# Optimization experiments

Measured on AMD Instinct MI355X. Metric: run time of the kernel, lower is better.

## Reference

```python
import jax, jax.numpy as jnp
import numpy as np

N_NODES = 50000
N_EDGES = 800000
H_NODE = 128
H_EDGE = 128
EPS = 1e-5


def _bn(x, gamma, beta):
    # training-mode BatchNorm1d over axis 0 (biased variance)
    mean = jnp.mean(x, axis=0)
    var = jnp.var(x, axis=0)
    return (x - mean) * jax.lax.rsqrt(var + EPS) * gamma + beta


def setup_inputs() -> dict:
    key = jax.random.key(0)
    ks = jax.random.split(key, 8)
    d_in = H_NODE + H_EDGE          # 256
    d_out = 2 * H_NODE              # 256
    bound = 1.0 / np.sqrt(d_in)
    return {
        "node_emb": jax.random.normal(ks[0], (N_NODES, H_NODE), jnp.float32),
        "edge_emb": jax.random.normal(ks[1], (N_EDGES, H_EDGE), jnp.float32),
        "i": jax.random.randint(ks[2], (N_EDGES,), 0, N_NODES, jnp.int64),
        "w1": jax.random.uniform(ks[3], (d_out, d_in), jnp.float32, -bound, bound),
        "b1": jax.random.uniform(ks[4], (d_out,), jnp.float32, -bound, bound),
        "g1": jnp.ones((d_out,), jnp.float32),
        "be1": jnp.zeros((d_out,), jnp.float32),
        "g2": jnp.ones((H_NODE,), jnp.float32),
        "be2": jnp.zeros((H_NODE,), jnp.float32),
    }


def reference(node_emb, edge_emb, i, w1, b1, g1, be1, g2, be2):
    # gather + concat: [E, H_NODE + H_EDGE]
    c1 = jnp.concatenate([node_emb[i], edge_emb], axis=1)
    # linear -> BN: [E, 2*H_NODE]
    c1 = _bn(c1 @ w1.T + b1, g1, be1)
    c1_filter, c1_core = jnp.split(c1, 2, axis=1)
    msg = jax.nn.sigmoid(c1_filter) * jnp.tanh(c1_core)  # [E, H_NODE]
    # scatter-sum back to nodes
    c1_emb = jax.ops.segment_sum(msg, i, num_segments=node_emb.shape[0])
    c1_emb = _bn(c1_emb, g2, be2)
    return jnp.tanh(node_emb + c1_emb)
```

## Files before the change

kernel.cpp:

```cpp
#include <hip/hip_runtime.h>
#include <hip/hip_fp16.h>
#include <cstdint>
#include <cstddef>

#define NN 50000
#define NE 800000
#define EPSV 1e-5f
#define NTILES (NE / 128)
#define EGRID 768

typedef _Float16 f16_t;
typedef f16_t f16x8 __attribute__((ext_vector_type(8)));
typedef f16_t f16x4 __attribute__((ext_vector_type(4)));
typedef f16_t f16x2 __attribute__((ext_vector_type(2)));
typedef float f32x4 __attribute__((ext_vector_type(4)));

__device__ __forceinline__ float fast_tanh(float x) {
  float e2 = __expf(2.f * x);
  return 1.f - 2.f / (e2 + 1.f);
}
__device__ __forceinline__ float fast_sigmoid(float x) {
  return 1.f / (1.f + __expf(-x));
}

__launch_bounds__(256, 4)
__global__ void node_proj(const float* __restrict__ A, const float* __restrict__ w1,
                          const float* __restrict__ b1, f16_t* __restrict__ P) {
  __shared__ f16_t Alds[128][136];
  const int tid = threadIdx.x;
  const int wave = tid >> 6;
  const int lane = tid & 63;
  const int quad = lane >> 4;
  const int l16 = lane & 15;

  int cols[4];
#pragma unroll
  for (int nt = 0; nt < 4; ++nt) cols[nt] = 16 * wave + 64 * nt + l16;

  f16x8 bfrag[4][4];
#pragma unroll
  for (int nt = 0; nt < 4; ++nt)
#pragma unroll
    for (int ks = 0; ks < 4; ++ks) {
      const float* src = w1 + (size_t)cols[nt] * 256 + ks * 32 + quad * 8;
#pragma unroll
      for (int j = 0; j < 8; ++j) bfrag[nt][ks][j] = (f16_t)src[j];
    }

  float c0[4];
#pragma unroll
  for (int nt = 0; nt < 4; ++nt) c0[nt] = b1[cols[nt]];

  const int row0 = blockIdx.x * 128;
  {
    const int r = tid >> 1, half = tid & 1;
    const int grow = row0 + r;
    f16_t* dst = &Alds[r][half * 64];
    if (grow < NN) {
      const float4* src = (const float4*)(A + (size_t)grow * 128 + half * 64);
#pragma unroll
      for (int c = 0; c < 8; ++c) {
        float4 v0 = src[2 * c], v1 = src[2 * c + 1];
        f16x8 pk = {(f16_t)v0.x, (f16_t)v0.y, (f16_t)v0.z, (f16_t)v0.w,
                    (f16_t)v1.x, (f16_t)v1.y, (f16_t)v1.z, (f16_t)v1.w};
        *(f16x8*)(dst + c * 8) = pk;
      }
    } else {
      f16x8 z = {0, 0, 0, 0, 0, 0, 0, 0};
#pragma unroll
      for (int c = 0; c < 8; ++c) *(f16x8*)(dst + c * 8) = z;
    }
  }
  __syncthreads();

#pragma unroll 1
  for (int m = 0; m < 8; ++m) {
    f16x8 afrag[4];
#pragma unroll
    for (int ks = 0; ks < 4; ++ks)
      afrag[ks] = *(const f16x8*)&Alds[m * 16 + l16][ks * 32 + quad * 8];
    f32x4 acc[4];
#pragma unroll
    for (int nt = 0; nt < 4; ++nt) acc[nt] = (f32x4){0.f, 0.f, 0.f, 0.f};
#pragma unroll
    for (int ks = 0; ks < 4; ++ks)
#pragma unroll
      for (int nt = 0; nt < 4; ++nt)
        acc[nt] = __builtin_amdgcn_mfma_f32_16x16x32_f16(
            afrag[ks], bfrag[nt][ks], acc[nt], 0, 0, 0);
    const int rbase = row0 + m * 16 + quad * 4;
#pragma unroll
    for (int reg = 0; reg < 4; ++reg) {
      int g = rbase + reg;
      if (g < NN) {
        f16x2 pA, pB;
        pA[0] = (f16_t)(acc[0][reg] + c0[0]);
        pA[1] = (f16_t)(acc[2][reg] + c0[2]);
        pB[0] = (f16_t)(acc[1][reg] + c0[1]);
        pB[1] = (f16_t)(acc[3][reg] + c0[3]);
        *(f16x2*)&P[(size_t)g * 256 + wave * 32 + l16 * 2] = pA;
        *(f16x2*)&P[(size_t)g * 256 + (wave + 4) * 32 + l16 * 2] = pB;
      }
    }
  }
}

template <int MODE>
__launch_bounds__(512, 6)
__global__ void edge_pass(const float* __restrict__ A, const float* __restrict__ w1,
                          const int* __restrict__ idx, const f16_t* __restrict__ P,
                          float* __restrict__ stats, const float* __restrict__ st,
                          f16_t* __restrict__ outp, int* __restrict__ ctr) {
  __shared__ f16_t Alds[128][136];
  __shared__ int sIdx[128];
  __shared__ int s_tile;
  const int tid = threadIdx.x;
  const int w = tid >> 6;
  const int lane = tid & 63;
  const int quad = lane >> 4;
  const int l16 = lane & 15;

  int cols[2];
#pragma unroll
  for (int n = 0; n < 2; ++n) cols[n] = 16 * w + 128 * n + l16;

  f16x8 bfrag[2][4];
#pragma unroll
  for (int n = 0; n < 2; ++n)
#pragma unroll
    for (int ks = 0; ks < 4; ++ks) {
      const float* src = w1 + (size_t)cols[n] * 256 + 128 + ks * 32 + quad * 8;
#pragma unroll
      for (int j = 0; j < 8; ++j) bfrag[n][ks][j] = (f16_t)src[j];
    }

  float c0[2], c1c[2];
  if (MODE == 2) {
#pragma unroll
    for (int n = 0; n < 2; ++n) {
      c0[n] = st[cols[n]];
      c1c[n] = st[256 + cols[n]];
    }
  }
  float ssum[2] = {0.f, 0.f};
  float ssq[2] = {0.f, 0.f};

  for (;;) {
    if (tid == 0) s_tile = atomicAdd(ctr, 1);
    __syncthreads();
    const int t = s_tile;
    if (t >= NTILES) break;
    const int row0 = t * 128;

    if (tid < 128) sIdx[tid] = idx[row0 + tid];
    {
      const int r = tid >> 2, q4 = tid & 3;
      const float4* src = (const float4*)(A + (size_t)(row0 + r) * 128 + q4 * 32);
      f16_t* dst = &Alds[r][q4 * 32];
#pragma unroll
      for (int c = 0; c < 4; ++c) {
        float4 v0 = src[2 * c], v1 = src[2 * c + 1];
        f16x8 pk = {(f16_t)v0.x, (f16_t)v0.y, (f16_t)v0.z, (f16_t)v0.w,
                    (f16_t)v1.x, (f16_t)v1.y, (f16_t)v1.z, (f16_t)v1.w};
        *(f16x8*)(dst + c * 8) = pk;
      }
    }
    __syncthreads();

    int nodeC[4];
    f16x2 pvC[4];
#pragma unroll
    for (int reg = 0; reg < 4; ++reg) {
      nodeC[reg] = sIdx[quad * 4 + reg];
      pvC[reg] = *(const f16x2*)&P[(size_t)nodeC[reg] * 256 + w * 32 + l16 * 2];
    }

#pragma unroll 1
    for (int m = 0; m < 8; ++m) {
      const int mm = (m + 1) & 7;
      int nodeN[4];
      f16x2 pvN[4];
#pragma unroll
      for (int reg = 0; reg < 4; ++reg) {
        nodeN[reg] = sIdx[mm * 16 + quad * 4 + reg];
        pvN[reg] = *(const f16x2*)&P[(size_t)nodeN[reg] * 256 + w * 32 + l16 * 2];
      }

      f16x8 afrag[4];
#pragma unroll
      for (int ks = 0; ks < 4; ++ks)
        afrag[ks] = *(const f16x8*)&Alds[m * 16 + l16][ks * 32 + quad * 8];

      f32x4 acc[2];
      acc[0] = (f32x4){0.f, 0.f, 0.f, 0.f};
      acc[1] = (f32x4){0.f, 0.f, 0.f, 0.f};
      __builtin_amdgcn_s_setprio(1);
#pragma unroll
      for (int ks = 0; ks < 4; ++ks) {
        acc[0] = __builtin_amdgcn_mfma_f32_16x16x32_f16(afrag[ks], bfrag[0][ks],
                                                        acc[0], 0, 0, 0);
        acc[1] = __builtin_amdgcn_mfma_f32_16x16x32_f16(afrag[ks], bfrag[1][ks],
                                                        acc[1], 0, 0, 0);
      }
      __builtin_amdgcn_s_setprio(0);

#pragma unroll
      for (int reg = 0; reg < 4; ++reg) {
        const float h0 = acc[0][reg] + (float)pvC[reg][0];
        const float h1 = acc[1][reg] + (float)pvC[reg][1];
        if (MODE == 2) {
          const float hn0 = h0 * c0[0] + c1c[0];
          const float hn1 = h1 * c0[1] + c1c[1];
          const float msg = fast_sigmoid(hn0) * fast_tanh(hn1);
          const float o = __shfl_xor(msg, 1);
          if ((l16 & 1) == 0) {
            f16x2 val;
            val[0] = (f16_t)msg;
            val[1] = (f16_t)o;
            __half2* addr =
                (__half2*)&outp[(size_t)nodeC[reg] * 128 + 16 * w + (l16 & ~1)];
            unsafeAtomicAdd(addr, *(__half2*)&val);
          }
        } else {
          ssum[0] += h0; ssq[0] += h0 * h0;
          ssum[1] += h1; ssq[1] += h1 * h1;
          if (MODE == 3) {
            f16x2 hp = {(f16_t)h0, (f16_t)h1};
            const int edge = row0 + m * 16 + quad * 4 + reg;
            *(f16x2*)&outp[(size_t)edge * 256 + w * 32 + l16 * 2] = hp;
          }
        }
      }
#pragma unroll
      for (int reg = 0; reg < 4; ++reg) {
        nodeC[reg] = nodeN[reg];
        pvC[reg] = pvN[reg];
      }
    }
    __syncthreads();
  }

  if (MODE != 2) {
#pragma unroll
    for (int n = 0; n < 2; ++n) {
      float s = ssum[n], q = ssq[n];
      s += __shfl_xor(s, 16); s += __shfl_xor(s, 32);
      q += __shfl_xor(q, 16); q += __shfl_xor(q, 32);
      if (quad == 0) {
        atomicAdd(&stats[cols[n]], s);
        atomicAdd(&stats[256 + cols[n]], q);
      }
    }
  }
}

__global__ void finalize1(const float* __restrict__ stats, const float* __restrict__ g1,
                          const float* __restrict__ be1, float* __restrict__ st,
                          float* __restrict__ st_sw) {
  int j = threadIdx.x;
  float mean = stats[j] * (1.f / NE);
  float var = stats[256 + j] * (1.f / NE) - mean * mean;
  float s = g1[j] * rsqrtf(var + EPSV);
  float t = be1[j] - mean * s;
  st[j] = s;
  st[256 + j] = t;
  int wq = (j >> 4) & 7, n = j >> 7, lj = j & 15;
  int pos = wq * 32 + lj * 2 + n;
  st_sw[pos] = s;
  st_sw[256 + pos] = t;
}

__launch_bounds__(256, 8)
__global__ void edge_apply(const f16_t* __restrict__ hsw, const int* __restrict__ idx,
                           const float* __restrict__ stw, f16_t* __restrict__ acc16) {
  const int i = blockIdx.x * 256 + threadIdx.x;
  const int e = i >> 5;
  const int k2 = i & 31;
  const int node = idx[e];
  const int w = k2 >> 3, lp = k2 & 7;
  const f16x4 ha = *(const f16x4*)&hsw[(size_t)e * 256 + w * 32 + lp * 4];
  const f16x4 hb = *(const f16x4*)&hsw[(size_t)e * 256 + (w + 4) * 32 + lp * 4];
  const float4 sA = *(const float4*)&stw[w * 32 + lp * 4];
  const float4 sB = *(const float4*)&stw[(w + 4) * 32 + lp * 4];
  const float4 tA = *(const float4*)&stw[256 + w * 32 + lp * 4];
  const float4 tB = *(const float4*)&stw[256 + (w + 4) * 32 + lp * 4];
  f16x2 va, vb;
  va[0] = (f16_t)(fast_sigmoid((float)ha[0] * sA.x + tA.x) *
                  fast_tanh((float)ha[1] * sA.y + tA.y));
  va[1] = (f16_t)(fast_sigmoid((float)ha[2] * sA.z + tA.z) *
                  fast_tanh((float)ha[3] * sA.w + tA.w));
  vb[0] = (f16_t)(fast_sigmoid((float)hb[0] * sB.x + tB.x) *
                  fast_tanh((float)hb[1] * sB.y + tB.y));
  vb[1] = (f16_t)(fast_sigmoid((float)hb[2] * sB.z + tB.z) *
                  fast_tanh((float)hb[3] * sB.w + tB.w));
  const int cA = 16 * w + 2 * lp;
  f16_t* rowp = acc16 + (size_t)node * 128;
  unsafeAtomicAdd((__half2*)(rowp + cA), *(__half2*)&va);
  unsafeAtomicAdd((__half2*)(rowp + 64 + cA), *(__half2*)&vb);
}

__global__ void bn2_stats(const f16_t* __restrict__ acc16, float* __restrict__ stats) {
  const int tid = threadIdx.x;
  const int c2 = tid & 63;
  const int ph = tid >> 6;
  float s0 = 0.f, s1 = 0.f, q0 = 0.f, q1 = 0.f;
  for (int row = blockIdx.x * 4 + ph; row < NN; row += gridDim.x * 4) {
    f16x2 v = *(const f16x2*)&acc16[(size_t)row * 128 + 2 * c2];
    float a = (float)v[0], b = (float)v[1];
    s0 += a; q0 += a * a;
    s1 += b; q1 += b * b;
  }
  __shared__ float red[256][4];
  red[tid][0] = s0; red[tid][1] = s1; red[tid][2] = q0; red[tid][3] = q1;
  __syncthreads();
  if (ph == 0) {
    float a0 = 0.f, a1 = 0.f, b0 = 0.f, b1 = 0.f;
#pragma unroll
    for (int p = 0; p < 4; ++p) {
      a0 += red[p * 64 + c2][0]; a1 += red[p * 64 + c2][1];
      b0 += red[p * 64 + c2][2]; b1 += red[p * 64 + c2][3];
    }
    atomicAdd(&stats[2 * c2], a0);
    atomicAdd(&stats[2 * c2 + 1], a1);
    atomicAdd(&stats[128 + 2 * c2], b0);
    atomicAdd(&stats[128 + 2 * c2 + 1], b1);
  }
}

__global__ void final_kernel(const float* __restrict__ node_emb,
                             const float* __restrict__ bn2sums,
                             const float* __restrict__ g2, const float* __restrict__ be2,
                             const f16_t* __restrict__ acc16, float* __restrict__ out) {
  int i = blockIdx.x * blockDim.x + threadIdx.x;
  if (i >= NN * 32) return;
  int c4 = i & 31;
  int row = i >> 5;
  float4 sm = ((const float4*)bn2sums)[c4];
  float4 sq = ((const float4*)(bn2sums + 128))[c4];
  float4 g = ((const float4*)g2)[c4];
  float4 b = ((const float4*)be2)[c4];
  float4 s4, h4;
  {
    float mean, var;
    mean = sm.x * (1.f / NN); var = sq.x * (1.f / NN) - mean * mean;
    s4.x = g.x * rsqrtf(var + EPSV); h4.x = b.x - mean * s4.x;
    mean = sm.y * (1.f / NN); var = sq.y * (1.f / NN) - mean * mean;
    s4.y = g.y * rsqrtf(var + EPSV); h4.y = b.y - mean * s4.y;
    mean = sm.z * (1.f / NN); var = sq.z * (1.f / NN) - mean * mean;
    s4.z = g.z * rsqrtf(var + EPSV); h4.z = b.z - mean * s4.z;
    mean = sm.w * (1.f / NN); var = sq.w * (1.f / NN) - mean * mean;
    s4.w = g.w * rsqrtf(var + EPSV); h4.w = b.w - mean * s4.w;
  }
  float4 ne = ((const float4*)node_emb)[i];
  f16x4 cv = *(const f16x4*)&acc16[(size_t)row * 128 + c4 * 4];
  float4 r;
  r.x = fast_tanh(ne.x + (float)cv[0] * s4.x + h4.x);
  r.y = fast_tanh(ne.y + (float)cv[1] * s4.y + h4.y);
  r.z = fast_tanh(ne.z + (float)cv[2] * s4.z + h4.z);
  r.w = fast_tanh(ne.w + (float)cv[3] * s4.w + h4.w);
  ((float4*)out)[i] = r;
}

extern "C" void kernel_launch(void* const* d_in, const int* in_sizes, int n_in,
                              void* d_out, int out_size, void* d_ws, size_t ws_size,
                              hipStream_t stream) {
  (void)in_sizes; (void)n_in; (void)out_size;
  const float* node_emb = (const float*)d_in[0];
  const float* edge_emb = (const float*)d_in[1];
  const int* idx = (const int*)d_in[2];
  const float* w1 = (const float*)d_in[3];
  const float* b1 = (const float*)d_in[4];
  const float* g1 = (const float*)d_in[5];
  const float* be1 = (const float*)d_in[6];
  const float* g2 = (const float*)d_in[7];
  const float* be2 = (const float*)d_in[8];
  float* out = (float*)d_out;

  float* wsf = (float*)d_ws;
  float* bn1sums = wsf;
  float* st = wsf + 512;
  float* bn2sums = wsf + 1024;
  int* ctr1 = (int*)(wsf + 1536);
  int* ctr2 = (int*)(wsf + 1537);
  float* st_sw = wsf + 2048;
  char* base = (char*)d_ws + 16384;
  f16_t* P = (f16_t*)base;
  f16_t* acc16 = (f16_t*)(base + (size_t)NN * 512);
  f16_t* hsw = (f16_t*)(base + (size_t)NN * 512 + (size_t)NN * 256);
  const size_t need_h = 16384 + (size_t)NN * 512 + (size_t)NN * 256 + (size_t)NE * 512;

  hipMemsetAsync(wsf, 0, 2560 * sizeof(float), stream);
  hipMemsetAsync(acc16, 0, (size_t)NN * 256, stream);

  node_proj<<<(NN + 127) / 128, 256, 0, stream>>>(node_emb, w1, b1, P);
  if (ws_size >= need_h) {
    edge_pass<3><<<EGRID, 512, 0, stream>>>(edge_emb, w1, idx, P, bn1sums, nullptr,
                                            hsw, ctr1);
    finalize1<<<1, 256, 0, stream>>>(bn1sums, g1, be1, st, st_sw);
    edge_apply<<<NE * 32 / 256, 256, 0, stream>>>(hsw, idx, st_sw, acc16);
  } else {
    edge_pass<1><<<EGRID, 512, 0, stream>>>(edge_emb, w1, idx, P, bn1sums, nullptr,
                                            nullptr, ctr1);
    finalize1<<<1, 256, 0, stream>>>(bn1sums, g1, be1, st, st_sw);
    edge_pass<2><<<EGRID, 512, 0, stream>>>(edge_emb, w1, idx, P, bn1sums, st,
                                            acc16, ctr2);
  }
  bn2_stats<<<256, 256, 0, stream>>>(acc16, bn2sums);
  final_kernel<<<(NN * 32 + 255) / 256, 256, 0, stream>>>(node_emb, bn2sums, g2,
                                                          be2, acc16, out);
}
```

Baseline: 911.7 us.

## Replace atomic scatter with CSR-grouped segment reduction into LDS

Builds a CSR edge list sorted by destination node (count, single-block scan, fill) and adds an apply2 kernel where each block owns 64 nodes, gathers their edges' pre-BN activations, applies BN, gate and tanh, and accumulates into shared memory before writing fp16 results once. This is meant to remove global atomic scatter contention and the acc16 memset. In exchange it adds three small kernels plus a serial 1024-thread scan, irregular gathers of hsw rows, and load imbalance across nodes. The path is only taken when the workspace is large enough.

After: 1.176 ms. +29.0%, slower.

```diff
diff --git a/kernel.cpp b/kernel.cpp
--- a/kernel.cpp
+++ b/kernel.cpp
@@ -8,6 +8,8 @@
 #define EPSV 1e-5f
 #define NTILES (NE / 128)
 #define EGRID 768
+#define SCAN_T 1024
+#define CHUNK ((NN + SCAN_T - 1) / SCAN_T)
 
 typedef _Float16 f16_t;
 typedef f16_t f16x8 __attribute__((ext_vector_type(8)));
@@ -57,10 +59,10 @@
     const int grow = row0 + r;
     f16_t* dst = &Alds[r][half * 64];
     if (grow < NN) {
-      const float4* src = (const float4*)(A + (size_t)grow * 128 + half * 64);
+      const f32x4* src = (const f32x4*)(A + (size_t)grow * 128 + half * 64);
 #pragma unroll
       for (int c = 0; c < 8; ++c) {
-        float4 v0 = src[2 * c], v1 = src[2 * c + 1];
+        f32x4 v0 = src[2 * c], v1 = src[2 * c + 1];
         f16x8 pk = {(f16_t)v0.x, (f16_t)v0.y, (f16_t)v0.z, (f16_t)v0.w,
                     (f16_t)v1.x, (f16_t)v1.y, (f16_t)v1.z, (f16_t)v1.w};
         *(f16x8*)(dst + c * 8) = pk;
@@ -155,11 +157,11 @@
     if (tid < 128) sIdx[tid] = idx[row0 + tid];
     {
       const int r = tid >> 2, q4 = tid & 3;
-      const float4* src = (const float4*)(A + (size_t)(row0 + r) * 128 + q4 * 32);
+      const f32x4* src = (const f32x4*)(A + (size_t)(row0 + r) * 128 + q4 * 32);
       f16_t* dst = &Alds[r][q4 * 32];
 #pragma unroll
       for (int c = 0; c < 4; ++c) {
-        float4 v0 = src[2 * c], v1 = src[2 * c + 1];
+        f32x4 v0 = src[2 * c], v1 = src[2 * c + 1];
         f16x8 pk = {(f16_t)v0.x, (f16_t)v0.y, (f16_t)v0.z, (f16_t)v0.w,
                     (f16_t)v1.x, (f16_t)v1.y, (f16_t)v1.z, (f16_t)v1.w};
         *(f16x8*)(dst + c * 8) = pk;
@@ -268,6 +270,116 @@
   int pos = wq * 32 + lj * 2 + n;
   st_sw[pos] = s;
   st_sw[256 + pos] = t;
+}
+
+__global__ void csr_count(const int* __restrict__ idx, int* __restrict__ cnt) {
+  int i = blockIdx.x * 256 + threadIdx.x;
+  if (i < NE / 4) {
+    int4 v = ((const int4*)idx)[i];
+    atomicAdd(&cnt[v.x], 1);
+    atomicAdd(&cnt[v.y], 1);
+    atomicAdd(&cnt[v.z], 1);
+    atomicAdd(&cnt[v.w], 1);
+  }
+}
+
+__global__ void csr_scan(const int* __restrict__ cnt, int* __restrict__ off,
+                         int* __restrict__ cur) {
+  __shared__ int ls[SCAN_T];
+  const int t = threadIdx.x;
+  const int b0 = t * CHUNK;
+  int s = 0;
+  for (int k = 0; k < CHUNK; ++k) {
+    int n = b0 + k;
+    if (n < NN) s += cnt[n];
+  }
+  ls[t] = s;
+  __syncthreads();
+  for (int d = 1; d < SCAN_T; d <<= 1) {
+    int u = (t >= d) ? ls[t - d] : 0;
+    __syncthreads();
+    ls[t] += u;
+    __syncthreads();
+  }
+  int run = ls[t] - s;
+  for (int k = 0; k < CHUNK; ++k) {
+    int n = b0 + k;
+    if (n < NN) {
+      off[n] = run;
+      cur[n] = run;
+      run += cnt[n];
+    }
+  }
+  if (t == SCAN_T - 1) off[NN] = run;
+}
+
+__global__ void csr_fill(const int* __restrict__ idx, int* __restrict__ cur,
+                         int* __restrict__ elist) {
+  int i = blockIdx.x * 256 + threadIdx.x;
+  if (i < NE / 4) {
+    int4 v = ((const int4*)idx)[i];
+    int e = 4 * i;
+    elist[atomicAdd(&cur[v.x], 1)] = (e)     | ((v.x & 63) << 20);
+    elist[atomicAdd(&cur[v.y], 1)] = (e + 1) | ((v.y & 63) << 20);
+    elist[atomicAdd(&cur[v.z], 1)] = (e + 2) | ((v.z & 63) << 20);
+    elist[atomicAdd(&cur[v.w], 1)] = (e + 3) | ((v.w & 63) << 20);
+  }
+}
+
+__launch_bounds__(256, 4)
+__global__ void apply2(const f16_t* __restrict__ hsw, const int* __restrict__ off,
+                       const int* __restrict__ elist, const float* __restrict__ stw,
+                       f16_t* __restrict__ acc16) {
+  __shared__ float accL[64 * 128];
+  const int tid = threadIdx.x;
+  const int wv = tid >> 6;
+  const int lane = tid & 63;
+  const int n0 = blockIdx.x * 64;
+
+  for (int i = tid; i < 64 * 128; i += 256) accL[i] = 0.f;
+
+  const float4 sv = *(const float4*)&stw[lane * 4];
+  const float4 tv = *(const float4*)&stw[256 + lane * 4];
+  const int c0 = 16 * (lane >> 3) + ((lane & 7) << 1);
+  __syncthreads();
+
+  int na = n0 + 16 * wv;
+  int nb = na + 16;
+  if (na > NN) na = NN;
+  if (nb > NN) nb = NN;
+  const int jbeg = (na <= NN) ? off[na] : NE;
+  const int jend = (nb <= NN) ? off[nb] : NE;
+
+  for (int jb = jbeg; jb < jend; jb += 64) {
+    const int nent = (jend - jb < 64) ? (jend - jb) : 64;
+    int ent = (jb + lane < jend) ? elist[jb + lane] : 0;
+#pragma unroll 4
+    for (int j = 0; j < nent; ++j) {
+      const int en = __shfl(ent, j);
+      const int e = en & 0xFFFFF;
+      const int ln = en >> 20;
+      const f16x4 h = *(const f16x4*)&hsw[(size_t)e * 256 + lane * 4];
+      const float m0 = fast_sigmoid((float)h[0] * sv.x + tv.x) *
+                       fast_tanh((float)h[1] * sv.y + tv.y);
+      const float m1 = fast_sigmoid((float)h[2] * sv.z + tv.z) *
+                       fast_tanh((float)h[3] * sv.w + tv.w);
+      float* p = &accL[ln * 128 + c0];
+      p[0] += m0;
+      p[1] += m1;
+    }
+  }
+  __syncthreads();
+
+  const int cp = tid & 63;
+  const int g = tid >> 6;
+  for (int r = g * 16; r < g * 16 + 16; ++r) {
+    const int n = n0 + r;
+    if (n >= NN) break;
+    f16x2 o;
+    o[0] = (f16_t)accL[r * 128 + 2 * cp];
+    o[1] = (f16_t)accL[r * 128 + 2 * cp + 1];
+    *(f16x2*)&acc16[(size_t)n * 128 + 2 * cp] = o;
+  }
 }
 
 __launch_bounds__(256, 8)
@@ -387,18 +499,34 @@
   f16_t* P = (f16_t*)base;
   f16_t* acc16 = (f16_t*)(base + (size_t)NN * 512);
   f16_t* hsw = (f16_t*)(base + (size_t)NN * 512 + (size_t)NN * 256);
+  int* cnt = (int*)(base + (size_t)NN * 512 + (size_t)NN * 256 + (size_t)NE * 512);
+  int* off = cnt + NN;
+  int* cur = off + NN + 1;
+  int* elist = cur + NN;
+
   const size_t need_h = 16384 + (size_t)NN * 512 + (size_t)NN * 256 + (size_t)NE * 512;
+  const size_t need_full = need_h + sizeof(int) * (size_t)(3 * NN + 1 + NE);
 
   hipMemsetAsync(wsf, 0, 2560 * sizeof(float), stream);
-  hipMemsetAsync(acc16, 0, (size_t)NN * 256, stream);
 
   node_proj<<<(NN + 127) / 128, 256, 0, stream>>>(node_emb, w1, b1, P);
-  if (ws_size >= need_h) {
+  if (ws_size >= need_full) {
+    hipMemsetAsync(cnt, 0, sizeof(int) * NN, stream);
+    csr_count<<<(NE / 4 + 255) / 256, 256, 0, stream>>>(idx, cnt);
+    csr_scan<<<1, SCAN_T, 0, stream>>>(cnt, off, cur);
+    csr_fill<<<(NE / 4 + 255) / 256, 256, 0, stream>>>(idx, cur, elist);
+    edge_pass<3><<<EGRID, 512, 0, stream>>>(edge_emb, w1, idx, P, bn1sums, nullptr,
+                                            hsw, ctr1);
+    finalize1<<<1, 256, 0, stream>>>(bn1sums, g1, be1, st, st_sw);
+    apply2<<<(NN + 63) / 64, 256, 0, stream>>>(hsw, off, elist, st_sw, acc16);
+  } else if (ws_size >= need_h) {
+    hipMemsetAsync(acc16, 0, (size_t)NN * 256, stream);
     edge_pass<3><<<EGRID, 512, 0, stream>>>(edge_emb, w1, idx, P, bn1sums, nullptr,
                                             hsw, ctr1);
     finalize1<<<1, 256, 0, stream>>>(bn1sums, g1, be1, st, st_sw);
     edge_apply<<<NE * 32 / 256, 256, 0, stream>>>(hsw, idx, st_sw, acc16);
   } else {
+    hipMemsetAsync(acc16, 0, (size_t)NN * 256, stream);
     edge_pass<1><<<EGRID, 512, 0, stream>>>(edge_emb, w1, idx, P, bn1sums, nullptr,
                                             nullptr, ctr1);
     finalize1<<<1, 256, 0, stream>>>(bn1sums, g1, be1, st, st_sw);
```

## Prefetch next edge tile into registers while computing current tile

Applied to the files above, without the earlier changes.

The persistent edge_pass loop now claims the next tile early and issues its global loads for edge embeddings and indices into registers right after the LDS write barrier, so they overlap with the MFMA and gather work on the current tile. The trailing barrier is removed because the next iteration's barrier now separates the LDS writes. This costs 32 extra VGPRs per thread for the prefetch buffer, which may reduce occupancy under launch_bounds(512,6). Dropping the end-of-loop sync could also race on Alds or s_nx if some waves are still reading the current tile.

After: 1.106 ms. +21.3%, slower.

```diff
diff --git a/kernel.cpp b/kernel.cpp
--- a/kernel.cpp
+++ b/kernel.cpp
@@ -57,10 +57,10 @@
     const int grow = row0 + r;
     f16_t* dst = &Alds[r][half * 64];
     if (grow < NN) {
-      const float4* src = (const float4*)(A + (size_t)grow * 128 + half * 64);
+      const f32x4* src = (const f32x4*)(A + (size_t)grow * 128 + half * 64);
 #pragma unroll
       for (int c = 0; c < 8; ++c) {
-        float4 v0 = src[2 * c], v1 = src[2 * c + 1];
+        f32x4 v0 = src[2 * c], v1 = src[2 * c + 1];
         f16x8 pk = {(f16_t)v0.x, (f16_t)v0.y, (f16_t)v0.z, (f16_t)v0.w,
                     (f16_t)v1.x, (f16_t)v1.y, (f16_t)v1.z, (f16_t)v1.w};
         *(f16x8*)(dst + c * 8) = pk;
@@ -113,12 +113,13 @@
                           f16_t* __restrict__ outp, int* __restrict__ ctr) {
   __shared__ f16_t Alds[128][136];
   __shared__ int sIdx[128];
-  __shared__ int s_tile;
+  __shared__ int s_nx;
   const int tid = threadIdx.x;
   const int w = tid >> 6;
   const int lane = tid & 63;
   const int quad = lane >> 4;
   const int l16 = lane & 15;
+  const int sr = tid >> 2, sq4 = tid & 3;
 
   int cols[2];
 #pragma unroll
@@ -145,27 +146,44 @@
   float ssum[2] = {0.f, 0.f};
   float ssq[2] = {0.f, 0.f};
 
-  for (;;) {
-    if (tid == 0) s_tile = atomicAdd(ctr, 1);
+  f32x4 sv[8];
+  int idreg = 0;
+
+  if (tid == 0) s_nx = atomicAdd(ctr, 1);
+  __syncthreads();
+  int t = s_nx;
+  if (t < NTILES) {
+    const f32x4* src = (const f32x4*)(A + (size_t)(t * 128 + sr) * 128 + sq4 * 32);
+#pragma unroll
+    for (int c = 0; c < 8; ++c) sv[c] = src[c];
+    if (tid < 128) idreg = idx[t * 128 + tid];
+  }
+
+  while (t < NTILES) {
+    if (tid == 0) s_nx = atomicAdd(ctr, 1);
     __syncthreads();
-    const int t = s_tile;
-    if (t >= NTILES) break;
-    const int row0 = t * 128;
-
-    if (tid < 128) sIdx[tid] = idx[row0 + tid];
+    const int tn = s_nx;
     {
-      const int r = tid >> 2, q4 = tid & 3;
-      const float4* src = (const float4*)(A + (size_t)(row0 + r) * 128 + q4 * 32);
-      f16_t* dst = &Alds[r][q4 * 32];
+      f16_t* dst = &Alds[sr][sq4 * 32];
 #pragma unroll
       for (int c = 0; c < 4; ++c) {
-        float4 v0 = src[2 * c], v1 = src[2 * c + 1];
+        f32x4 v0 = sv[2 * c], v1 = sv[2 * c + 1];
         f16x8 pk = {(f16_t)v0.x, (f16_t)v0.y, (f16_t)v0.z, (f16_t)v0.w,
                     (f16_t)v1.x, (f16_t)v1.y, (f16_t)v1.z, (f16_t)v1.w};
         *(f16x8*)(dst + c * 8) = pk;
       }
+      if (tid < 128) sIdx[tid] = idreg;
     }
     __syncthreads();
+
+    if (tn < NTILES) {
+      const f32x4* src = (const f32x4*)(A + (size_t)(tn * 128 + sr) * 128 + sq4 * 32);
+#pragma unroll
+      for (int c = 0; c < 8; ++c) sv[c] = src[c];
+      if (tid < 128) idreg = idx[tn * 128 + tid];
+    }
+
+    const int row0 = t * 128;
 
     int nodeC[4];
     f16x2 pvC[4];
@@ -237,7 +255,7 @@
         pvC[reg] = pvN[reg];
       }
     }
-    __syncthreads();
+    t = tn;
   }
 
   if (MODE != 2) {
```
